# Performance work log

Measured on AMD Instinct MI355X. Metric: run time of the kernel, lower is better.

The kernel has to match this reference:

```python
import jax, jax.numpy as jnp
import numpy as np

T, IN_DIM, H1, H2 = 64, 84, 128, 84
BATCH = 8192


def _glorot(key, shape, fan):
    bound = 1.0 / np.sqrt(fan)
    return jax.random.uniform(key, shape, jnp.float32, -bound, bound)


def setup_inputs() -> dict:
    key = jax.random.key(0)
    ks = jax.random.split(key, 13)
    x = jax.random.normal(ks[0], (BATCH, T, IN_DIM, 1), jnp.float32)
    # rnn1 layer 0: 84 -> 128
    w_ih_l0 = _glorot(ks[1], (H1, IN_DIM), H1)
    w_hh_l0 = _glorot(ks[2], (H1, H1), H1)
    b_ih_l0 = _glorot(ks[3], (H1,), H1)
    b_hh_l0 = _glorot(ks[4], (H1,), H1)
    # rnn1 layer 1: 128 -> 128
    w_ih_l1 = _glorot(ks[5], (H1, H1), H1)
    w_hh_l1 = _glorot(ks[6], (H1, H1), H1)
    b_ih_l1 = _glorot(ks[7], (H1,), H1)
    b_hh_l1 = _glorot(ks[8], (H1,), H1)
    # rnn2: 128 -> 84
    w_ih_l2 = _glorot(ks[9], (H2, H1), H2)
    w_hh_l2 = _glorot(ks[10], (H2, H2), H2)
    b_ih_l2 = _glorot(ks[11], (H2,), H2)
    b_hh_l2 = _glorot(ks[12], (H2,), H2)
    return {
        "x": x,
        "w_ih_l0": w_ih_l0, "w_hh_l0": w_hh_l0, "b_ih_l0": b_ih_l0, "b_hh_l0": b_hh_l0,
        "w_ih_l1": w_ih_l1, "w_hh_l1": w_hh_l1, "b_ih_l1": b_ih_l1, "b_hh_l1": b_hh_l1,
        "w_ih_l2": w_ih_l2, "w_hh_l2": w_hh_l2, "b_ih_l2": b_ih_l2, "b_hh_l2": b_hh_l2,
    }


def _elman_layer(x, w_ih, w_hh, b_ih, b_hh):
    # x: (B, T, I) -> (B, T, H); h_t = tanh(x_t W_ih^T + b_ih + h_{t-1} W_hh^T + b_hh)
    # Precompute the input projection for all timesteps as one big GEMM.
    xp = jnp.einsum('bti,hi->bth', x, w_ih) + (b_ih + b_hh)  # (B, T, H)
    h0 = jnp.zeros((x.shape[0], w_hh.shape[0]), x.dtype)

    def step(h, xp_t):
        h = jnp.tanh(xp_t + h @ w_hh.T)
        return h, h

    _, ys = jax.lax.scan(step, h0, jnp.swapaxes(xp, 0, 1))  # (T, B, H)
    return jnp.swapaxes(ys, 0, 1)


def reference(x,
              w_ih_l0, w_hh_l0, b_ih_l0, b_hh_l0,
              w_ih_l1, w_hh_l1, b_ih_l1, b_hh_l1,
              w_ih_l2, w_hh_l2, b_ih_l2, b_hh_l2):
    x_ = jnp.squeeze(x, -1)                                   # (B, 64, 84)
    h = _elman_layer(x_, w_ih_l0, w_hh_l0, b_ih_l0, b_hh_l0)  # (B, 64, 128)
    h = _elman_layer(h, w_ih_l1, w_hh_l1, b_ih_l1, b_hh_l1)   # (B, 64, 128)
    h = _elman_layer(h, w_ih_l2, w_hh_l2, b_ih_l2, b_hh_l2)   # (B, 64, 84)
    return h[..., None]                                       # (B, 64, 84, 1)
```

## Files before the change

kernel.cpp:

```cpp
#include <hip/hip_runtime.h>


typedef __bf16 bf16x8 __attribute__((ext_vector_type(8)));
typedef float  f32x4  __attribute__((ext_vector_type(4)));
typedef float  f32x16 __attribute__((ext_vector_type(16)));
typedef unsigned short u16;
typedef unsigned int   u32;
typedef u16 u16x8 __attribute__((ext_vector_type(8)));
typedef u16 u16x4 __attribute__((ext_vector_type(4)));

#define MFMA32(a, b, c) __builtin_amdgcn_mfma_f32_32x32x16_bf16((a), (b), (c), 0, 0, 0)

__device__ __forceinline__ float bf2f(u16 v) {
    return __builtin_bit_cast(float, (u32)v << 16);
}
__device__ __forceinline__ u16 f2bf(float f) {
    u32 u = __builtin_bit_cast(u32, f);
    u = u + 0x7fffu + ((u >> 16) & 1u);
    return (u16)(u >> 16);
}
__device__ __forceinline__ float tanh_fast(float x) {
    float xc = fminf(fmaxf(x, -12.f), 12.f);
    float e  = __expf(2.f * xc);
    return (e - 1.f) * __builtin_amdgcn_rcpf(e + 1.f);
}
__device__ __forceinline__ bf16x8 ld_lds8(const u16* p) {
    return __builtin_bit_cast(bf16x8, *(const u16x8*)p);
}
__device__ __forceinline__ int aswz(int row, int off) {
    return row * 128 + (off ^ ((row & 7) << 3));
}
__device__ __forceinline__ void store4_hl(u16* ph, u16* pl, f32x4 v) {
    u16x4 hi, lo;
#pragma unroll
    for (int j = 0; j < 4; j++) {
        u16 h = f2bf(v[j]);
        hi[j] = h;
        lo[j] = f2bf(v[j] - bf2f(h));
    }
    *(u16x4*)ph = hi;
    *(u16x4*)pl = lo;
}

struct fragp { bf16x8 h, l; };

__device__ __forceinline__ fragp load_wfrag_hl(const float* W, int Hr, int Kr,
                                               int n, int kbase) {
    u16x8 uh = {0,0,0,0,0,0,0,0}, ul = {0,0,0,0,0,0,0,0};
    if (n < Hr) {
#pragma unroll
        for (int j = 0; j < 8; j++) {
            int k = kbase + j;
            if (k < Kr) {
                float w = W[n * Kr + k];
                u16 hi = f2bf(w);
                uh[j] = hi;
                ul[j] = f2bf(w - bf2f(hi));
            }
        }
    }
    fragp r;
    r.h = __builtin_bit_cast(bf16x8, uh);
    r.l = __builtin_bit_cast(bf16x8, ul);
    return r;
}

__device__ __forceinline__ f32x16 mm3t(const fragp& w, bf16x8 ah, bf16x8 al, f32x16 c) {
    c = MFMA32(w.h, ah, c);
    c = MFMA32(w.l, ah, c);
    c = MFMA32(w.h, al, c);
    return c;
}

#define STG_ISSUE(trr)                                                   \
    {                                                                    \
        const int tofs = (trr) * 84;                                     \
        xq0 = *(const f32x4*)&xg[goffq0 + tofs];                         \
        if (tid_s < 160) xq1 = *(const f32x4*)&xg[goffq1 + tofs];        \
    }
#define STG_WRITE(PNv)                                                   \
    {                                                                    \
        u16* bh = &xbh[(PNv)][0];                                        \
        u16* bl = &xbl[(PNv)][0];                                        \
        store4_hl(&bh[lofsq0], &bl[lofsq0], xq0);                        \
        if (tid_s < 160) store4_hl(&bh[lofsq1], &bl[lofsq1], xq1);       \
    }
#define STG_SETUP()                                                      \
    int goffq0, lofsq0, goffq1, lofsq1;                                  \
    {                                                                    \
        int r0 = tid_s / 21, c0 = (tid_s - r0 * 21) * 4;                 \
        goffq0 = r0 * 5376 + c0;                                         \
        lofsq0 = r0 * 128 + (c0 ^ ((r0 & 7) << 3));                      \
        int s1 = tid_s + 512, r1 = s1 / 21, c1 = (s1 - r1 * 21) * 4;     \
        goffq1 = r1 * 5376 + c1;                                         \
        lofsq1 = r1 * 128 + (c1 ^ ((r1 & 7) << 3));                      \
    }                                                                    \
    f32x4 xq0, xq1;

__global__ __launch_bounds__(768, 3)
void rnn_fused(const float* __restrict__ x,
               const float* __restrict__ wih0, const float* __restrict__ whh0,
               const float* __restrict__ bih0, const float* __restrict__ bhh0,
               const float* __restrict__ wih1, const float* __restrict__ whh1,
               const float* __restrict__ bih1, const float* __restrict__ bhh1,
               const float* __restrict__ wih2, const float* __restrict__ whh2,
               const float* __restrict__ bih2, const float* __restrict__ bhh2,
               float* __restrict__ out)
{
    __shared__ __align__(16) u16 h0h[2][4096], h0l[2][4096];
    __shared__ __align__(16) u16 h1h[2][4096], h1l[2][4096];
    __shared__ __align__(16) u16 h2h[2][4096], h2l[2][4096];
    __shared__ __align__(16) u16 xbh[2][4096], xbl[2][4096];
    __shared__ float biasF[3][128];

    const int tid  = threadIdx.x;
    const int wv   = tid >> 6;
    const int lane = tid & 63;
    const int mrow = lane & 31;
    const int q2   = lane >> 5;
    const int kq   = q2 * 8;
    const int q4   = q2 * 4;
    const int b0   = blockIdx.x * 32;
    const float* xg = x + (long)b0 * 5376;

    { u16* z = &h0h[0][0]; for (int i = tid; i < 4096; i += 768) z[i] = 0; }
    { u16* z = &h0l[0][0]; for (int i = tid; i < 4096; i += 768) z[i] = 0; }
    { u16* z = &h1h[1][0]; for (int i = tid; i < 4096; i += 768) z[i] = 0; }
    { u16* z = &h1l[1][0]; for (int i = tid; i < 4096; i += 768) z[i] = 0; }
    { u16* z = &h2h[0][0]; for (int i = tid; i < 4096; i += 768) z[i] = 0; }
    { u16* z = &h2l[0][0]; for (int i = tid; i < 4096; i += 768) z[i] = 0; }
    { u16* z = &xbh[0][0]; for (int i = tid; i < 8192; i += 768) z[i] = 0; }
    { u16* z = &xbl[0][0]; for (int i = tid; i < 8192; i += 768) z[i] = 0; }
    for (int s = tid; s < 672; s += 768) {
        int row = s / 21, cq = (s - row * 21) * 4;
        f32x4 v = *(const f32x4*)&xg[(long)row * 5376 + cq];
        int idx = row * 128 + (cq ^ ((row & 7) << 3));
        store4_hl(&xbh[0][idx], &xbl[0][idx], v);
    }
    for (int i = tid; i < 384; i += 768) {
        int l = i >> 7, n = i & 127;
        float v = 0.f;
        if (l == 0)      v = bih0[n] + bhh0[n];
        else if (l == 1) v = bih1[n] + bhh1[n];
        else if (n < 84) v = bih2[n] + bhh2[n];
        biasF[l][n] = v;
    }
    __syncthreads();

    if (wv < 4) {
        const int nb = wv * 32;
        fragp fih0[6], fhh0[8];
#pragma unroll
        for (int c = 0; c < 6; c++)
            fih0[c] = load_wfrag_hl(wih0, 128, 84, nb + mrow, c * 16 + kq);
#pragma unroll
        for (int c = 0; c < 8; c++)
            fhh0[c] = load_wfrag_hl(whh0, 128, 128, nb + mrow, c * 16 + kq);
        const int tid_s = wv * 64 + lane;
        STG_SETUP();

        for (int rr = 0; rr < 66; ++rr) {
            const int P = rr & 1, PN = P ^ 1;
            if (rr <= 62) STG_ISSUE(rr + 1);
            if (rr <= 63) {
                f32x16 accA, accB;
#pragma unroll
                for (int g = 0; g < 4; g++) {
                    f32x4 v = *(const f32x4*)&biasF[0][nb + g * 8 + q4];
                    accA[4*g+0] = v[0]; accA[4*g+1] = v[1];
                    accA[4*g+2] = v[2]; accA[4*g+3] = v[3];
                }
#pragma unroll
                for (int i = 0; i < 16; i++) accB[i] = 0.f;
                __builtin_amdgcn_s_setprio(1);
#pragma unroll
                for (int c = 0; c < 6; c++) {
                    const int idx = aswz(mrow, c * 16 + kq);
                    bf16x8 ah = ld_lds8(&xbh[P][idx]), al = ld_lds8(&xbl[P][idx]);
                    if (c & 1) accA = mm3t(fih0[c], ah, al, accA);
                    else       accB = mm3t(fih0[c], ah, al, accB);
                }
#pragma unroll
                for (int c = 0; c < 8; c++) {
                    const int idx = aswz(mrow, c * 16 + kq);
                    bf16x8 ah = ld_lds8(&h0h[P][idx]), al = ld_lds8(&h0l[P][idx]);
                    if (c & 1) accA = mm3t(fhh0[c], ah, al, accA);
                    else       accB = mm3t(fhh0[c], ah, al, accB);
                }
                __builtin_amdgcn_s_setprio(0);
                f32x16 acc = accA + accB;
#pragma unroll
                for (int g = 0; g < 4; g++) {
                    const int col = nb + g * 8 + q4;
                    f32x4 v;
                    v[0] = tanh_fast(acc[4*g+0]); v[1] = tanh_fast(acc[4*g+1]);
                    v[2] = tanh_fast(acc[4*g+2]); v[3] = tanh_fast(acc[4*g+3]);
                    const int idx = mrow * 128 + (col ^ ((mrow & 7) << 3));
                    store4_hl(&h0h[PN][idx], &h0l[PN][idx], v);
                }
            }
            if (rr <= 62) STG_WRITE(PN);
            __syncthreads();
        }
    } else if (wv < 8) {
        const int nb = (wv - 4) * 32;
        fragp fih1[8], fhh1[8];
#pragma unroll
        for (int c = 0; c < 8; c++) {
            fih1[c] = load_wfrag_hl(wih1, 128, 128, nb + mrow, c * 16 + kq);
            fhh1[c] = load_wfrag_hl(whh1, 128, 128, nb + mrow, c * 16 + kq);
        }
        for (int rr = 0; rr < 66; ++rr) {
            const int P = rr & 1, PN = P ^ 1;
            if (rr >= 1 && rr <= 64) {
                f32x16 accA, accB;
#pragma unroll
                for (int g = 0; g < 4; g++) {
                    f32x4 v = *(const f32x4*)&biasF[1][nb + g * 8 + q4];
                    accA[4*g+0] = v[0]; accA[4*g+1] = v[1];
                    accA[4*g+2] = v[2]; accA[4*g+3] = v[3];
                }
#pragma unroll
                for (int i = 0; i < 16; i++) accB[i] = 0.f;
                __builtin_amdgcn_s_setprio(1);
#pragma unroll
                for (int c = 0; c < 8; c++) {
                    const int idx = aswz(mrow, c * 16 + kq);
                    bf16x8 ah = ld_lds8(&h0h[P][idx]), al = ld_lds8(&h0l[P][idx]);
                    if (c & 1) accA = mm3t(fih1[c], ah, al, accA);
                    else       accB = mm3t(fih1[c], ah, al, accB);
                }
#pragma unroll
                for (int c = 0; c < 8; c++) {
                    const int idx = aswz(mrow, c * 16 + kq);
                    bf16x8 ah = ld_lds8(&h1h[P][idx]), al = ld_lds8(&h1l[P][idx]);
                    if (c & 1) accA = mm3t(fhh1[c], ah, al, accA);
                    else       accB = mm3t(fhh1[c], ah, al, accB);
                }
                __builtin_amdgcn_s_setprio(0);
                f32x16 acc = accA + accB;
#pragma unroll
                for (int g = 0; g < 4; g++) {
                    const int col = nb + g * 8 + q4;
                    f32x4 v;
                    v[0] = tanh_fast(acc[4*g+0]); v[1] = tanh_fast(acc[4*g+1]);
                    v[2] = tanh_fast(acc[4*g+2]); v[3] = tanh_fast(acc[4*g+3]);
                    const int idx = mrow * 128 + (col ^ ((mrow & 7) << 3));
                    store4_hl(&h1h[PN][idx], &h1l[PN][idx], v);
                }
            }
            __syncthreads();
        }
    } else if (wv < 11) {
        const int nb = (wv - 8) * 32;
        fragp fih2[8], fhh2[6];
#pragma unroll
        for (int c = 0; c < 8; c++)
            fih2[c] = load_wfrag_hl(wih2, 84, 128, nb + mrow, c * 16 + kq);
#pragma unroll
        for (int c = 0; c < 6; c++)
            fhh2[c] = load_wfrag_hl(whh2, 84, 84, nb + mrow, c * 16 + kq);
        const int tid_s = (wv - 4) * 64 + lane;
        STG_SETUP();

        for (int rr = 0; rr < 66; ++rr) {
            const int P = rr & 1, PN = P ^ 1;
            if (rr <= 62) STG_ISSUE(rr + 1);
            if (rr >= 2) {
                const int t2 = rr - 2;
                f32x16 accA, accB;
#pragma unroll
                for (int g = 0; g < 4; g++) {
                    f32x4 v = *(const f32x4*)&biasF[2][nb + g * 8 + q4];
                    accA[4*g+0] = v[0]; accA[4*g+1] = v[1];
                    accA[4*g+2] = v[2]; accA[4*g+3] = v[3];
                }
#pragma unroll
                for (int i = 0; i < 16; i++) accB[i] = 0.f;
                __builtin_amdgcn_s_setprio(1);
#pragma unroll
                for (int c = 0; c < 8; c++) {
                    const int idx = aswz(mrow, c * 16 + kq);
                    bf16x8 ah = ld_lds8(&h1h[P][idx]), al = ld_lds8(&h1l[P][idx]);
                    if (c & 1) accA = mm3t(fih2[c], ah, al, accA);
                    else       accB = mm3t(fih2[c], ah, al, accB);
                }
#pragma unroll
                for (int c = 0; c < 6; c++) {
                    const int idx = aswz(mrow, c * 16 + kq);
                    bf16x8 ah = ld_lds8(&h2h[P][idx]), al = ld_lds8(&h2l[P][idx]);
                    if (c & 1) accA = mm3t(fhh2[c], ah, al, accA);
                    else       accB = mm3t(fhh2[c], ah, al, accB);
                }
                __builtin_amdgcn_s_setprio(0);
                f32x16 acc = accA + accB;
#pragma unroll
                for (int g = 0; g < 4; g++) {
                    const int col = nb + g * 8 + q4;
                    f32x4 v;
                    v[0] = tanh_fast(acc[4*g+0]); v[1] = tanh_fast(acc[4*g+1]);
                    v[2] = tanh_fast(acc[4*g+2]); v[3] = tanh_fast(acc[4*g+3]);
                    const int idx = mrow * 128 + (col ^ ((mrow & 7) << 3));
                    store4_hl(&h2h[PN][idx], &h2l[PN][idx], v);
                    if (col < 84)
                        *(f32x4*)(out + (long)(b0 + mrow) * 5376 + t2 * 84 + col) = v;
                }
            }
            if (rr <= 62) STG_WRITE(PN);
            __syncthreads();
        }
    } else {
        const int tid_s = 7 * 64 + lane;
        STG_SETUP();
        for (int rr = 0; rr < 66; ++rr) {
            const int PN = (rr & 1) ^ 1;
            if (rr <= 62) STG_ISSUE(rr + 1);
            if (rr <= 62) STG_WRITE(PN);
            __syncthreads();
        }
    }
}

extern "C" void kernel_launch(void* const* d_in, const int* in_sizes, int n_in,
                              void* d_out, int out_size, void* d_ws, size_t ws_size,
                              hipStream_t stream) {
    (void)in_sizes; (void)n_in; (void)out_size; (void)d_ws; (void)ws_size;
    const float* x    = (const float*)d_in[0];
    const float* wih0 = (const float*)d_in[1];
    const float* whh0 = (const float*)d_in[2];
    const float* bih0 = (const float*)d_in[3];
    const float* bhh0 = (const float*)d_in[4];
    const float* wih1 = (const float*)d_in[5];
    const float* whh1 = (const float*)d_in[6];
    const float* bih1 = (const float*)d_in[7];
    const float* bhh1 = (const float*)d_in[8];
    const float* wih2 = (const float*)d_in[9];
    const float* whh2 = (const float*)d_in[10];
    const float* bih2 = (const float*)d_in[11];
    const float* bhh2 = (const float*)d_in[12];
    float* out = (float*)d_out;

    rnn_fused<<<dim3(8192 / 32), dim3(768), 0, stream>>>(
        x, wih0, whh0, bih0, bhh0, wih1, whh1, bih1, bhh1,
        wih2, whh2, bih2, bhh2, out);
}
```

Baseline: 592.6 us.

## Switch to 16x16x32 MFMA with 16-row batch tiles and doubled grid

Each block now handles 16 batch rows instead of 32, and the grid doubles to 512 blocks so more CUs get work, given the 256-block grid before. The matrix ops use 16x16x32 bf16 MFMA, with two 16-column output fragments per wave in place of one 32x32 tile. LDS buffers shrink by half and biases go into registers, which lets launch bounds ask for higher occupancy. The x-staging work is redistributed away from the layer-2 waves. The trade-off is that each block repeats the serial 66-step recurrence and reloads its weights with less MFMA work per step.

```diff
diff --git a/kernel.cpp b/kernel.cpp
--- a/kernel.cpp
+++ b/kernel.cpp
@@ -3,13 +3,12 @@
 
 typedef __bf16 bf16x8 __attribute__((ext_vector_type(8)));
 typedef float  f32x4  __attribute__((ext_vector_type(4)));
-typedef float  f32x16 __attribute__((ext_vector_type(16)));
 typedef unsigned short u16;
 typedef unsigned int   u32;
 typedef u16 u16x8 __attribute__((ext_vector_type(8)));
 typedef u16 u16x4 __attribute__((ext_vector_type(4)));
 
-#define MFMA32(a, b, c) __builtin_amdgcn_mfma_f32_32x32x16_bf16((a), (b), (c), 0, 0, 0)
+#define MFMA16(a, b, c) __builtin_amdgcn_mfma_f32_16x16x32_bf16((a), (b), (c), 0, 0, 0)
 
 __device__ __forceinline__ float bf2f(u16 v) {
     return __builtin_bit_cast(float, (u32)v << 16);
@@ -40,6 +39,12 @@
     }
     *(u16x4*)ph = hi;
     *(u16x4*)pl = lo;
+}
+__device__ __forceinline__ f32x4 tanh4(f32x4 a) {
+    f32x4 r;
+#pragma unroll
+    for (int j = 0; j < 4; j++) r[j] = tanh_fast(a[j]);
+    return r;
 }
 
 struct fragp { bf16x8 h, l; };
@@ -65,39 +70,36 @@
     return r;
 }
 
-__device__ __forceinline__ f32x16 mm3t(const fragp& w, bf16x8 ah, bf16x8 al, f32x16 c) {
-    c = MFMA32(w.h, ah, c);
-    c = MFMA32(w.l, ah, c);
-    c = MFMA32(w.h, al, c);
+__device__ __forceinline__ f32x4 mm3s(const fragp& w, bf16x8 ah, bf16x8 al, f32x4 c) {
+    c = MFMA16(w.h, ah, c);
+    c = MFMA16(w.l, ah, c);
+    c = MFMA16(w.h, al, c);
     return c;
 }
 
+#define STG_SETUP()                                                      \
+    int g0o, l0o, g1o, l1o;                                              \
+    const bool has1 = (sid < 16);                                        \
+    {                                                                    \
+        int r0 = sid / 21, c0 = (sid - r0 * 21) * 4;                     \
+        g0o = r0 * 5376 + c0; l0o = aswz(r0, c0);                        \
+        int s1 = sid + 320, r1 = s1 / 21, c1 = (s1 - r1 * 21) * 4;       \
+        g1o = r1 * 5376 + c1; l1o = aswz(r1, c1);                        \
+    }                                                                    \
+    f32x4 xq0, xq1;
 #define STG_ISSUE(trr)                                                   \
     {                                                                    \
         const int tofs = (trr) * 84;                                     \
-        xq0 = *(const f32x4*)&xg[goffq0 + tofs];                         \
-        if (tid_s < 160) xq1 = *(const f32x4*)&xg[goffq1 + tofs];        \
+        xq0 = *(const f32x4*)&xg[g0o + tofs];                            \
+        if (has1) xq1 = *(const f32x4*)&xg[g1o + tofs];                  \
     }
 #define STG_WRITE(PNv)                                                   \
     {                                                                    \
-        u16* bh = &xbh[(PNv)][0];                                        \
-        u16* bl = &xbl[(PNv)][0];                                        \
-        store4_hl(&bh[lofsq0], &bl[lofsq0], xq0);                        \
-        if (tid_s < 160) store4_hl(&bh[lofsq1], &bl[lofsq1], xq1);       \
-    }
-#define STG_SETUP()                                                      \
-    int goffq0, lofsq0, goffq1, lofsq1;                                  \
-    {                                                                    \
-        int r0 = tid_s / 21, c0 = (tid_s - r0 * 21) * 4;                 \
-        goffq0 = r0 * 5376 + c0;                                         \
-        lofsq0 = r0 * 128 + (c0 ^ ((r0 & 7) << 3));                      \
-        int s1 = tid_s + 512, r1 = s1 / 21, c1 = (s1 - r1 * 21) * 4;     \
-        goffq1 = r1 * 5376 + c1;                                         \
-        lofsq1 = r1 * 128 + (c1 ^ ((r1 & 7) << 3));                      \
-    }                                                                    \
-    f32x4 xq0, xq1;
-
-__global__ __launch_bounds__(768, 3)
+        store4_hl(&xbh[(PNv)][l0o], &xbl[(PNv)][l0o], xq0);              \
+        if (has1) store4_hl(&xbh[(PNv)][l1o], &xbl[(PNv)][l1o], xq1);    \
+    }
+
+__global__ __launch_bounds__(768, 6)
 void rnn_fused(const float* __restrict__ x,
                const float* __restrict__ wih0, const float* __restrict__ whh0,
                const float* __restrict__ bih0, const float* __restrict__ bhh0,
@@ -107,96 +109,83 @@
                const float* __restrict__ bih2, const float* __restrict__ bhh2,
                float* __restrict__ out)
 {
-    __shared__ __align__(16) u16 h0h[2][4096], h0l[2][4096];
-    __shared__ __align__(16) u16 h1h[2][4096], h1l[2][4096];
-    __shared__ __align__(16) u16 h2h[2][4096], h2l[2][4096];
-    __shared__ __align__(16) u16 xbh[2][4096], xbl[2][4096];
-    __shared__ float biasF[3][128];
+    __shared__ __align__(16) u16 h0h[2][2048], h0l[2][2048];
+    __shared__ __align__(16) u16 h1h[2][2048], h1l[2][2048];
+    __shared__ __align__(16) u16 h2h[2][2048], h2l[2][2048];
+    __shared__ __align__(16) u16 xbh[2][2048], xbl[2][2048];
 
     const int tid  = threadIdx.x;
     const int wv   = tid >> 6;
     const int lane = tid & 63;
-    const int mrow = lane & 31;
-    const int q2   = lane >> 5;
-    const int kq   = q2 * 8;
-    const int q4   = q2 * 4;
-    const int b0   = blockIdx.x * 32;
+    const int ln   = lane & 15;
+    const int q    = lane >> 4;
+    const int b0   = blockIdx.x * 16;
     const float* xg = x + (long)b0 * 5376;
 
-    { u16* z = &h0h[0][0]; for (int i = tid; i < 4096; i += 768) z[i] = 0; }
-    { u16* z = &h0l[0][0]; for (int i = tid; i < 4096; i += 768) z[i] = 0; }
-    { u16* z = &h1h[1][0]; for (int i = tid; i < 4096; i += 768) z[i] = 0; }
-    { u16* z = &h1l[1][0]; for (int i = tid; i < 4096; i += 768) z[i] = 0; }
-    { u16* z = &h2h[0][0]; for (int i = tid; i < 4096; i += 768) z[i] = 0; }
-    { u16* z = &h2l[0][0]; for (int i = tid; i < 4096; i += 768) z[i] = 0; }
-    { u16* z = &xbh[0][0]; for (int i = tid; i < 8192; i += 768) z[i] = 0; }
-    { u16* z = &xbl[0][0]; for (int i = tid; i < 8192; i += 768) z[i] = 0; }
-    for (int s = tid; s < 672; s += 768) {
-        int row = s / 21, cq = (s - row * 21) * 4;
-        f32x4 v = *(const f32x4*)&xg[(long)row * 5376 + cq];
-        int idx = row * 128 + (cq ^ ((row & 7) << 3));
+    for (int i = tid; i < 2048; i += 768) {
+        h0h[0][i] = 0; h0l[0][i] = 0;
+        h1h[1][i] = 0; h1l[1][i] = 0;
+        h2h[0][i] = 0; h2l[0][i] = 0;
+    }
+    { u16* z = &xbh[0][0]; for (int i = tid; i < 4096; i += 768) z[i] = 0; }
+    { u16* z = &xbl[0][0]; for (int i = tid; i < 4096; i += 768) z[i] = 0; }
+    __syncthreads();
+    for (int s = tid; s < 336; s += 768) {
+        int row = s / 21, col = (s - row * 21) * 4;
+        f32x4 v = *(const f32x4*)&xg[(long)row * 5376 + col];
+        int idx = aswz(row, col);
         store4_hl(&xbh[0][idx], &xbl[0][idx], v);
-    }
-    for (int i = tid; i < 384; i += 768) {
-        int l = i >> 7, n = i & 127;
-        float v = 0.f;
-        if (l == 0)      v = bih0[n] + bhh0[n];
-        else if (l == 1) v = bih1[n] + bhh1[n];
-        else if (n < 84) v = bih2[n] + bhh2[n];
-        biasF[l][n] = v;
     }
     __syncthreads();
 
     if (wv < 4) {
         const int nb = wv * 32;
-        fragp fih0[6], fhh0[8];
-#pragma unroll
-        for (int c = 0; c < 6; c++)
-            fih0[c] = load_wfrag_hl(wih0, 128, 84, nb + mrow, c * 16 + kq);
-#pragma unroll
-        for (int c = 0; c < 8; c++)
-            fhh0[c] = load_wfrag_hl(whh0, 128, 128, nb + mrow, c * 16 + kq);
-        const int tid_s = wv * 64 + lane;
+        fragp fih0[2][3], fhh0[2][4];
+#pragma unroll
+        for (int f = 0; f < 2; f++) {
+#pragma unroll
+            for (int c = 0; c < 3; c++)
+                fih0[f][c] = load_wfrag_hl(wih0, 128, 84, nb + f * 16 + ln, c * 32 + q * 8);
+#pragma unroll
+            for (int c = 0; c < 4; c++)
+                fhh0[f][c] = load_wfrag_hl(whh0, 128, 128, nb + f * 16 + ln, c * 32 + q * 8);
+        }
+        f32x4 bias0v[2];
+#pragma unroll
+        for (int f = 0; f < 2; f++) {
+            const int fb = nb + f * 16 + q * 4;
+            bias0v[f] = *(const f32x4*)&bih0[fb] + *(const f32x4*)&bhh0[fb];
+        }
+        const int sid = wv * 64 + lane;
         STG_SETUP();
 
         for (int rr = 0; rr < 66; ++rr) {
             const int P = rr & 1, PN = P ^ 1;
             if (rr <= 62) STG_ISSUE(rr + 1);
             if (rr <= 63) {
-                f32x16 accA, accB;
-#pragma unroll
-                for (int g = 0; g < 4; g++) {
-                    f32x4 v = *(const f32x4*)&biasF[0][nb + g * 8 + q4];
-                    accA[4*g+0] = v[0]; accA[4*g+1] = v[1];
-                    accA[4*g+2] = v[2]; accA[4*g+3] = v[3];
-                }
-#pragma unroll
-                for (int i = 0; i < 16; i++) accB[i] = 0.f;
+                f32x4 a0 = bias0v[0], a1 = bias0v[1];
                 __builtin_amdgcn_s_setprio(1);
 #pragma unroll
-                for (int c = 0; c < 6; c++) {
-                    const int idx = aswz(mrow, c * 16 + kq);
-                    bf16x8 ah = ld_lds8(&xbh[P][idx]), al = ld_lds8(&xbl[P][idx]);
-                    if (c & 1) accA = mm3t(fih0[c], ah, al, accA);
-                    else       accB = mm3t(fih0[c], ah, al, accB);
-                }
-#pragma unroll
-                for (int c = 0; c < 8; c++) {
-                    const int idx = aswz(mrow, c * 16 + kq);
-                    bf16x8 ah = ld_lds8(&h0h[P][idx]), al = ld_lds8(&h0l[P][idx]);
-                    if (c & 1) accA = mm3t(fhh0[c], ah, al, accA);
-                    else       accB = mm3t(fhh0[c], ah, al, accB);
+                for (int c = 0; c < 3; c++) {
+                    const int idx = aswz(ln, c * 32 + q * 8);
+                    bf16x8 bh = ld_lds8(&xbh[P][idx]), bl = ld_lds8(&xbl[P][idx]);
+                    a0 = mm3s(fih0[0][c], bh, bl, a0);
+                    a1 = mm3s(fih0[1][c], bh, bl, a1);
+                }
+#pragma unroll
+                for (int c = 0; c < 4; c++) {
+                    const int idx = aswz(ln, c * 32 + q * 8);
+                    bf16x8 bh = ld_lds8(&h0h[P][idx]), bl = ld_lds8(&h0l[P][idx]);
+                    a0 = mm3s(fhh0[0][c], bh, bl, a0);
+                    a1 = mm3s(fhh0[1][c], bh, bl, a1);
                 }
                 __builtin_amdgcn_s_setprio(0);
-                f32x16 acc = accA + accB;
-#pragma unroll
-                for (int g = 0; g < 4; g++) {
-                    const int col = nb + g * 8 + q4;
-                    f32x4 v;
-                    v[0] = tanh_fast(acc[4*g+0]); v[1] = tanh_fast(acc[4*g+1]);
-                    v[2] = tanh_fast(acc[4*g+2]); v[3] = tanh_fast(acc[4*g+3]);
-                    const int idx = mrow * 128 + (col ^ ((mrow & 7) << 3));
-                    store4_hl(&h0h[PN][idx], &h0l[PN][idx], v);
+                {
+                    f32x4 v0 = tanh4(a0), v1 = tanh4(a1);
+                    const int i0 = aswz(ln, nb + q * 4);
+                    const int i1 = aswz(ln, nb + 16 + q * 4);
+                    store4_hl(&h0h[PN][i0], &h0l[PN][i0], v0);
+                    store4_hl(&h0h[PN][i1], &h0l[PN][i1], v1);
                 }
             }
             if (rr <= 62) STG_WRITE(PN);
@@ -204,113 +193,106 @@
         }
     } else if (wv < 8) {
         const int nb = (wv - 4) * 32;
-        fragp fih1[8], fhh1[8];
-#pragma unroll
-        for (int c = 0; c < 8; c++) {
-            fih1[c] = load_wfrag_hl(wih1, 128, 128, nb + mrow, c * 16 + kq);
-            fhh1[c] = load_wfrag_hl(whh1, 128, 128, nb + mrow, c * 16 + kq);
+        fragp fih1[2][4], fhh1[2][4];
+#pragma unroll
+        for (int f = 0; f < 2; f++) {
+#pragma unroll
+            for (int c = 0; c < 4; c++) {
+                fih1[f][c] = load_wfrag_hl(wih1, 128, 128, nb + f * 16 + ln, c * 32 + q * 8);
+                fhh1[f][c] = load_wfrag_hl(whh1, 128, 128, nb + f * 16 + ln, c * 32 + q * 8);
+            }
+        }
+        f32x4 bias1v[2];
+#pragma unroll
+        for (int f = 0; f < 2; f++) {
+            const int fb = nb + f * 16 + q * 4;
+            bias1v[f] = *(const f32x4*)&bih1[fb] + *(const f32x4*)&bhh1[fb];
         }
         for (int rr = 0; rr < 66; ++rr) {
             const int P = rr & 1, PN = P ^ 1;
             if (rr >= 1 && rr <= 64) {
-                f32x16 accA, accB;
-#pragma unroll
-                for (int g = 0; g < 4; g++) {
-                    f32x4 v = *(const f32x4*)&biasF[1][nb + g * 8 + q4];
-                    accA[4*g+0] = v[0]; accA[4*g+1] = v[1];
-                    accA[4*g+2] = v[2]; accA[4*g+3] = v[3];
-                }
-#pragma unroll
-                for (int i = 0; i < 16; i++) accB[i] = 0.f;
+                f32x4 a0 = bias1v[0], a1 = bias1v[1];
                 __builtin_amdgcn_s_setprio(1);
 #pragma unroll
-                for (int c = 0; c < 8; c++) {
-                    const int idx = aswz(mrow, c * 16 + kq);
-                    bf16x8 ah = ld_lds8(&h0h[P][idx]), al = ld_lds8(&h0l[P][idx]);
-                    if (c & 1) accA = mm3t(fih1[c], ah, al, accA);
-                    else       accB = mm3t(fih1[c], ah, al, accB);
-                }
-#pragma unroll
-                for (int c = 0; c < 8; c++) {
-                    const int idx = aswz(mrow, c * 16 + kq);
-                    bf16x8 ah = ld_lds8(&h1h[P][idx]), al = ld_lds8(&h1l[P][idx]);
-                    if (c & 1) accA = mm3t(fhh1[c], ah, al, accA);
-                    else       accB = mm3t(fhh1[c], ah, al, accB);
+                for (int c = 0; c < 4; c++) {
+                    const int idx = aswz(ln, c * 32 + q * 8);
+                    bf16x8 bh = ld_lds8(&h0h[P][idx]), bl = ld_lds8(&h0l[P][idx]);
+                    a0 = mm3s(fih1[0][c], bh, bl, a0);
+                    a1 = mm3s(fih1[1][c], bh, bl, a1);
+                }
+#pragma unroll
+                for (int c = 0; c < 4; c++) {
+                    const int idx = aswz(ln, c * 32 + q * 8);
+                    bf16x8 bh = ld_lds8(&h1h[P][idx]), bl = ld_lds8(&h1l[P][idx]);
+                    a0 = mm3s(fhh1[0][c], bh, bl, a0);
+                    a1 = mm3s(fhh1[1][c], bh, bl, a1);
                 }
                 __builtin_amdgcn_s_setprio(0);
-                f32x16 acc = accA + accB;
-#pragma unroll
-                for (int g = 0; g < 4; g++) {
-                    const int col = nb + g * 8 + q4;
-                    f32x4 v;
-                    v[0] = tanh_fast(acc[4*g+0]); v[1] = tanh_fast(acc[4*g+1]);
-                    v[2] = tanh_fast(acc[4*g+2]); v[3] = tanh_fast(acc[4*g+3]);
-                    const int idx = mrow * 128 + (col ^ ((mrow & 7) << 3));
-                    store4_hl(&h1h[PN][idx], &h1l[PN][idx], v);
+                {
+                    f32x4 v0 = tanh4(a0), v1 = tanh4(a1);
+                    const int i0 = aswz(ln, nb + q * 4);
+                    const int i1 = aswz(ln, nb + 16 + q * 4);
+                    store4_hl(&h1h[PN][i0], &h1l[PN][i0], v0);
+                    store4_hl(&h1h[PN][i1], &h1l[PN][i1], v1);
                 }
             }
             __syncthreads();
         }
     } else if (wv < 11) {
         const int nb = (wv - 8) * 32;
-        fragp fih2[8], fhh2[6];
-#pragma unroll
-        for (int c = 0; c < 8; c++)
-            fih2[c] = load_wfrag_hl(wih2, 84, 128, nb + mrow, c * 16 + kq);
-#pragma unroll
-        for (int c = 0; c < 6; c++)
-            fhh2[c] = load_wfrag_hl(whh2, 84, 84, nb + mrow, c * 16 + kq);
-        const int tid_s = (wv - 4) * 64 + lane;
-        STG_SETUP();
-
+        fragp fih2[2][4], fhh2[2][3];
+#pragma unroll
+        for (int f = 0; f < 2; f++) {
+#pragma unroll
+            for (int c = 0; c < 4; c++)
+                fih2[f][c] = load_wfrag_hl(wih2, 84, 128, nb + f * 16 + ln, c * 32 + q * 8);
+#pragma unroll
+            for (int c = 0; c < 3; c++)
+                fhh2[f][c] = load_wfrag_hl(whh2, 84, 84, nb + f * 16 + ln, c * 32 + q * 8);
+        }
+        f32x4 bias2v[2];
+#pragma unroll
+        for (int f = 0; f < 2; f++) {
+            const int fb = nb + f * 16 + q * 4;
+            if (fb < 84) bias2v[f] = *(const f32x4*)&bih2[fb] + *(const f32x4*)&bhh2[fb];
+            else { bias2v[f][0]=0.f; bias2v[f][1]=0.f; bias2v[f][2]=0.f; bias2v[f][3]=0.f; }
+        }
         for (int rr = 0; rr < 66; ++rr) {
             const int P = rr & 1, PN = P ^ 1;
-            if (rr <= 62) STG_ISSUE(rr + 1);
             if (rr >= 2) {
                 const int t2 = rr - 2;
-                f32x16 accA, accB;
-#pragma unroll
-                for (int g = 0; g < 4; g++) {
-                    f32x4 v = *(const f32x4*)&biasF[2][nb + g * 8 + q4];
-                    accA[4*g+0] = v[0]; accA[4*g+1] = v[1];
-                    accA[4*g+2] = v[2]; accA[4*g+3] = v[3];
-                }
-#pragma unroll
-                for (int i = 0; i < 16; i++) accB[i] = 0.f;
+                f32x4 a0 = bias2v[0], a1 = bias2v[1];
                 __builtin_amdgcn_s_setprio(1);
 #pragma unroll
-                for (int c = 0; c < 8; c++) {
-                    const int idx = aswz(mrow, c * 16 + kq);
-                    bf16x8 ah = ld_lds8(&h1h[P][idx]), al = ld_lds8(&h1l[P][idx]);
-                    if (c & 1) accA = mm3t(fih2[c], ah, al, accA);
-                    else       accB = mm3t(fih2[c], ah, al, accB);
-                }
-#pragma unroll
-                for (int c = 0; c < 6; c++) {
-                    const int idx = aswz(mrow, c * 16 + kq);
-                    bf16x8 ah = ld_lds8(&h2h[P][idx]), al = ld_lds8(&h2l[P][idx]);
-                    if (c & 1) accA = mm3t(fhh2[c], ah, al, accA);
-                    else       accB = mm3t(fhh2[c], ah, al, accB);
+                for (int c = 0; c < 4; c++) {
+                    const int idx = aswz(ln, c * 32 + q * 8);
+                    bf16x8 bh = ld_lds8(&h1h[P][idx]), bl = ld_lds8(&h1l[P][idx]);
+                    a0 = mm3s(fih2[0][c], bh, bl, a0);
+                    a1 = mm3s(fih2[1][c], bh, bl, a1);
+                }
+#pragma unroll
+                for (int c = 0; c < 3; c++) {
+                    const int idx = aswz(ln, c * 32 + q * 8);
+                    bf16x8 bh = ld_lds8(&h2h[P][idx]), bl = ld_lds8(&h2l[P][idx]);
+                    a0 = mm3s(fhh2[0][c], bh, bl, a0);
+                    a1 = mm3s(fhh2[1][c], bh, bl, a1);
                 }
                 __builtin_amdgcn_s_setprio(0);
-                f32x16 acc = accA + accB;
-#pragma unroll
-                for (int g = 0; g < 4; g++) {
-                    const int col = nb + g * 8 + q4;
-                    f32x4 v;
-                    v[0] = tanh_fast(acc[4*g+0]); v[1] = tanh_fast(acc[4*g+1]);
-                    v[2] = tanh_fast(acc[4*g+2]); v[3] = tanh_fast(acc[4*g+3]);
-                    const int idx = mrow * 128 + (col ^ ((mrow & 7) << 3));
-                    store4_hl(&h2h[PN][idx], &h2l[PN][idx], v);
-                    if (col < 84)
-                        *(f32x4*)(out + (long)(b0 + mrow) * 5376 + t2 * 84 + col) = v;
-                }
-            }
-            if (rr <= 62) STG_WRITE(PN);
+                {
+                    f32x4 v0 = tanh4(a0), v1 = tanh4(a1);
+                    const int fb0 = nb + q * 4, fb1 = nb + 16 + q * 4;
+                    const int i0 = aswz(ln, fb0), i1 = aswz(ln, fb1);
+                    store4_hl(&h2h[PN][i0], &h2l[PN][i0], v0);
+                    store4_hl(&h2h[PN][i1], &h2l[PN][i1], v1);
+                    float* ob = out + (long)(b0 + ln) * 5376 + t2 * 84;
+                    if (fb0 < 84) *(f32x4*)(ob + fb0) = v0;
+                    if (fb1 < 84) *(f32x4*)(ob + fb1) = v1;
+                }
+            }
             __syncthreads();
         }
     } else {
-        const int tid_s = 7 * 64 + lane;
+        const int sid = 256 + lane;
         STG_SETUP();
         for (int rr = 0; rr < 66; ++rr) {
             const int PN = (rr & 1) ^ 1;
@@ -340,7 +322,7 @@
     const float* bhh2 = (const float*)d_in[12];
     float* out = (float*)d_out;
 
-    rnn_fused<<<dim3(8192 / 32), dim3(768), 0, stream>>>(
+    rnn_fused<<<dim3(8192 / 16), dim3(768), 0, stream>>>(
         x, wih0, whh0, bih0, bhh0, wih1, whh1, bih1, bhh1,
         wih2, whh2, bih2, bhh2, out);
 }
```

New measurement: 1.429 ms. 141% more time.
